# Performance work log

Hardware: AMD Instinct MI355X
Metric: run time of the kernel (lower is better)

Reference implementation:

```python
import jax, jax.numpy as jnp
import numpy as np

EPS = 1e-5

def rmsnorm(x, g):
    var = jnp.mean(jnp.square(x), axis=-1, keepdims=True)
    return x * jax.lax.rsqrt(var + EPS) * g

def setup_inputs() -> dict:
    key = jax.random.key(0)
    ks = jax.random.split(key, 8)
    B, S, T, D = 2, 2048, 2048, 1024
    H, HKV, HD = 16, 4, 64
    std = 0.02
    return {
        "x": jax.random.normal(ks[0], (B, S, D), jnp.float32),
        "kv": jax.random.normal(ks[1], (B, T, D), jnp.float32),
        "wq": jax.random.normal(ks[2], (H * HD, D), jnp.float32) * std,
        "wk": jax.random.normal(ks[3], (HKV * HD, D), jnp.float32) * std,
        "wv": jax.random.normal(ks[4], (HKV * HD, D), jnp.float32) * std,
        "wo": jax.random.normal(ks[5], (D, H * HD), jnp.float32) * std,
        "gq": jnp.ones((D,), jnp.float32),
        "gkv": jnp.ones((D,), jnp.float32),
    }

def reference(x, kv, wq, wk, wv, wo, gq, gkv):
    B, S, D = x.shape
    T = kv.shape[1]
    H, HKV, HD = 16, 4, 64
    R = H // HKV  # heads per kv group
    xn = rmsnorm(x, gq)
    kvn = rmsnorm(kv, gkv)
    # projections
    q = (xn @ wq.T).reshape(B, S, HKV, R, HD)   # grouped query heads
    k = (kvn @ wk.T).reshape(B, T, HKV, HD)
    v = (kvn @ wv.T).reshape(B, T, HKV, HD)
    scale = 1.0 / jnp.sqrt(jnp.float32(HD))
    # block-mask is None -> full dense cross attention; GQA via broadcast einsum
    scores = jnp.einsum('bsgrd,btgd->bgrst', q, k) * scale  # [B,HKV,R,S,T]
    probs = jax.nn.softmax(scores, axis=-1)
    out = jnp.einsum('bgrst,btgd->bsgrd', probs, v)  # [B,S,HKV,R,HD]
    out = out.reshape(B, S, H * HD) @ wo.T
    return x + out
```

## Files before the change

### kernel.cpp

```cpp
#include <hip/hip_runtime.h>

#define DEV __device__ __forceinline__

typedef __attribute__((ext_vector_type(8))) _Float16 h8;
typedef __attribute__((ext_vector_type(4))) float f32x4;

DEV unsigned short f2h(float f) {
  union { _Float16 h[2]; unsigned short u[2]; } v;
  v.h[0] = (_Float16)f;
  return v.u[0];
}

DEV float h2f(unsigned short u) {
  union { _Float16 h[2]; unsigned short u[2]; } v;
  v.u[0] = u;
  return (float)v.h[0];
}

DEV unsigned int pack2h(float a, float b) {
  union { __fp16 __attribute__((ext_vector_type(2))) p; unsigned int u; } v;
  v.p = __builtin_amdgcn_cvt_pkrtz(a, b);
  return v.u;
}

DEV void async_load16(const void* g, void* l) {
  __builtin_amdgcn_global_load_lds(
      (const __attribute__((address_space(1))) void*)g,
      (__attribute__((address_space(3))) void*)l,
      16, 0, 0);
}

__global__ __launch_bounds__(256) void prep(const float* __restrict__ x,
                                            const float* __restrict__ kv,
                                            const float* __restrict__ wq,
                                            const float* __restrict__ wk,
                                            const float* __restrict__ wv,
                                            const float* __restrict__ wo,
                                            const float* __restrict__ gq,
                                            const float* __restrict__ gkv,
                                            unsigned short* __restrict__ wqb,
                                            unsigned short* __restrict__ wkvb,
                                            unsigned short* __restrict__ wob,
                                            unsigned short* __restrict__ xn,
                                            unsigned short* __restrict__ kvn,
                                            float qscale) {
  const int b = blockIdx.x, tid = threadIdx.x;
  if (b < 2560) {
    const float* src;
    unsigned short* dst;
    float sc = 1.0f;
    int base;
    if (b < 1024) { src = wq; dst = wqb; sc = qscale; base = b; }
    else if (b < 1280) { src = wk; dst = wkvb; base = b - 1024; }
    else if (b < 1536) { src = wv; dst = wkvb + 262144; base = b - 1280; }
    else { src = wo; dst = wob; base = b - 1536; }
    const int i = (base * 256 + tid) * 4;
    float4 v = *(const float4*)&src[i];
    ushort4 o;
    o.x = f2h(v.x * sc); o.y = f2h(v.y * sc);
    o.z = f2h(v.z * sc); o.w = f2h(v.w * sc);
    *(ushort4*)&dst[i] = o;
    return;
  }
  int row = b - 2560;
  const float* src;
  const float* g;
  unsigned short* dst;
  if (row < 4096) { src = x; g = gq; dst = xn; }
  else { row -= 4096; src = kv; g = gkv; dst = kvn; }
  const float* xr = src + (size_t)row * 1024;
  float4 v = *(const float4*)&xr[tid * 4];
  float ss = v.x * v.x + v.y * v.y + v.z * v.z + v.w * v.w;
  ss += __shfl_xor(ss, 32); ss += __shfl_xor(ss, 16);
  ss += __shfl_xor(ss, 8);  ss += __shfl_xor(ss, 4);
  ss += __shfl_xor(ss, 2);  ss += __shfl_xor(ss, 1);
  __shared__ float red[4];
  if ((tid & 63) == 0) red[tid >> 6] = ss;
  __syncthreads();
  float tot = red[0] + red[1] + red[2] + red[3];
  float inv = rsqrtf(tot * (1.0f / 1024.0f) + 1e-5f);
  float4 gv = *(const float4*)&g[tid * 4];
  ushort4 o;
  o.x = f2h(v.x * inv * gv.x); o.y = f2h(v.y * inv * gv.y);
  o.z = f2h(v.z * inv * gv.z); o.w = f2h(v.w * inv * gv.w);
  *(ushort4*)&dst[(size_t)row * 1024 + tid * 4] = o;
}

#define GEMM_KLOOP(A_, W_, m0_, n0_, Al_, Bl_, acc_)                                   \
  for (int kk = 0; kk < 1024; kk += 64) {                                              \
    __syncthreads();                                                                   \
    _Pragma("unroll") for (int j = 0; j < 6; ++j) {                                    \
      const int idx = w * 6 + j;                                                       \
      if (idx < 16) {                                                                  \
        const int p = idx >> 3, rb = (idx & 7) * 16;                                   \
        async_load16(A_ + (size_t)(m0_ + rb + r4) * 1024 + kk + p * 32 + c4,           \
                     &Al_[p][rb * 32]);                                                \
      } else {                                                                         \
        const int ib = idx - 16;                                                       \
        const int p = ib >> 2, rb = (ib & 3) * 16;                                     \
        async_load16(W_ + (size_t)(n0_ + rb + r4) * 1024 + kk + p * 32 + c4,           \
                     &Bl_[p][rb * 32]);                                                \
      }                                                                                \
    }                                                                                  \
    __syncthreads();                                                                   \
    _Pragma("unroll") for (int kc = 0; kc < 2; ++kc) {                                 \
      h8 af[4], bf[2];                                                                 \
      _Pragma("unroll") for (int mi = 0; mi < 4; ++mi)                                 \
        af[mi] = *(const h8*)&Al_[kc][(wm0 + mi * 16 + ln) * 32 + quad * 8];           \
      _Pragma("unroll") for (int ni = 0; ni < 2; ++ni)                                 \
        bf[ni] = *(const h8*)&Bl_[kc][(wn0 + ni * 16 + ln) * 32 + quad * 8];           \
      _Pragma("unroll") for (int mi = 0; mi < 4; ++mi)                                 \
        _Pragma("unroll") for (int ni = 0; ni < 2; ++ni)                               \
          acc_[mi][ni] =                                                               \
              __builtin_amdgcn_mfma_f32_16x16x32_f16(af[mi], bf[ni], acc_[mi][ni],     \
                                                     0, 0, 0);                         \
    }                                                                                  \
  }

__global__ __launch_bounds__(256) void proj_gemm(const unsigned short* __restrict__ xn,
                                                 const unsigned short* __restrict__ kvn,
                                                 const unsigned short* __restrict__ wqb,
                                                 const unsigned short* __restrict__ wkvb,
                                                 unsigned short* __restrict__ qb,
                                                 unsigned short* __restrict__ kb,
                                                 unsigned short* __restrict__ vTb) {
  __shared__ unsigned short Al[2][128 * 32];
  __shared__ unsigned short Bl[2][64 * 32];
  const int tid = threadIdx.x;
  const int w = tid >> 6, l = tid & 63;
  const int quad = l >> 4, ln = l & 15;
  const int wm0 = (w >> 1) * 64, wn0 = (w & 1) * 32;
  const int r4 = l >> 2;
  const int c4 = (l & 3) * 8;

  int z = blockIdx.x;
  const unsigned short *A, *W;
  int m0, n0, isq;
  if (z < 512) { A = xn; W = wqb; m0 = (z >> 4) * 128; n0 = (z & 15) * 64; isq = 1; }
  else { z -= 512; A = kvn; W = wkvb; m0 = (z >> 3) * 128; n0 = (z & 7) * 64; isq = 0; }

  f32x4 acc[4][2] = {};
  GEMM_KLOOP(A, W, m0, n0, Al, Bl, acc)

#pragma unroll
  for (int mi = 0; mi < 4; ++mi)
#pragma unroll
    for (int ni = 0; ni < 2; ++ni)
#pragma unroll
      for (int r = 0; r < 4; ++r) {
        const int row = m0 + wm0 + mi * 16 + quad * 4 + r;
        const int col = n0 + wn0 + ni * 16 + ln;
        const unsigned short v = f2h(acc[mi][ni][r]);
        if (isq) {
          qb[((size_t)row << 10) + col] = v;
        } else if (col < 256) {
          kb[(size_t)row * 256 + col] = v;
        } else {
          const int c2 = col - 256, gg = c2 >> 6, dd = c2 & 63;
          const int bb = row >> 11, t = row & 2047;
          vTb[((size_t)((bb * 4 + gg) * 64 + dd) << 11) + t] = v;
        }
      }
}

__global__ __launch_bounds__(256) void o_gemm(const unsigned short* __restrict__ attb,
                                              const unsigned short* __restrict__ wob,
                                              const float* __restrict__ x,
                                              float* __restrict__ out) {
  __shared__ unsigned short Al[2][128 * 32];
  __shared__ unsigned short Bl[2][64 * 32];
  const int tid = threadIdx.x;
  const int w = tid >> 6, l = tid & 63;
  const int quad = l >> 4, ln = l & 15;
  const int wm0 = (w >> 1) * 64, wn0 = (w & 1) * 32;
  const int r4 = l >> 2;
  const int c4 = (l & 3) * 8;

  const int m0 = (blockIdx.x >> 4) * 128, n0 = (blockIdx.x & 15) * 64;

  f32x4 acc[4][2] = {};
  GEMM_KLOOP(attb, wob, m0, n0, Al, Bl, acc)

#pragma unroll
  for (int mi = 0; mi < 4; ++mi)
#pragma unroll
    for (int ni = 0; ni < 2; ++ni)
#pragma unroll
      for (int r = 0; r < 4; ++r) {
        const int row = m0 + wm0 + mi * 16 + quad * 4 + r;
        const int col = n0 + wn0 + ni * 16 + ln;
        const size_t idx = ((size_t)row << 10) + col;
        out[idx] = x[idx] + acc[mi][ni][r];
      }
}

__global__ __launch_bounds__(256, 4) void flash_attn(const unsigned short* __restrict__ q,
                                                     const unsigned short* __restrict__ k,
                                                     const unsigned short* __restrict__ vT,
                                                     unsigned short* __restrict__ o0,
                                                     unsigned short* __restrict__ o1,
                                                     float* __restrict__ l0p,
                                                     float* __restrict__ l1p) {
  __shared__ unsigned short KV[4][64 * 32];
  __shared__ unsigned short P[4 * 32 * 72];

  const int tid = threadIdx.x;
  const int w = tid >> 6, l = tid & 63;
  const int quad = l >> 4, ln = l & 15;
  const int s0 = blockIdx.x * 128;
  const int h = blockIdx.y, g = h >> 2;
  const int b = blockIdx.z >> 1, ts = blockIdx.z & 1;
  const int tbase = ts << 10;

  unsigned short* Opart = ts ? o1 : o0;
  float* lpart = ts ? l1p : l0p;

  h8 qf[2][2];
#pragma unroll
  for (int nq = 0; nq < 2; ++nq)
#pragma unroll
    for (int c = 0; c < 2; ++c)
      qf[nq][c] = *(const h8*)&q[(((size_t)(b * 2048 + s0 + w * 32 + nq * 16 + ln)) << 10) +
                                 h * 64 + c * 32 + quad * 8];

  f32x4 oacc[2][4] = {};
  float lsum[2] = {0.0f, 0.0f};

  const unsigned short* kbase = k + ((size_t)(b * 2048)) * 256 + g * 64;
  const unsigned short* vbase = vT + (((size_t)(b * 4 + g) * 64) << 11);
  unsigned short* Pw = &P[w * 32 * 72];

  const int r4 = l >> 2;
  const int c4 = (l & 3) * 8;

  for (int it = 0; it < 16; ++it) {
    const int t0 = tbase + it * 64;
    __syncthreads();
#pragma unroll
    for (int c = 0; c < 4; ++c) {
      const unsigned short* src;
      if (w < 2)
        src = kbase + (size_t)(t0 + c * 16 + r4) * 256 + w * 32 + c4;
      else
        src = vbase + (((size_t)(c * 16 + r4)) << 11) + t0 + (w - 2) * 32 + c4;
      async_load16(src, &KV[w][c * 512]);
    }
    __syncthreads();

    f32x4 st[2][4];
#pragma unroll
    for (int tb = 0; tb < 4; ++tb) {
      h8 ka = *(const h8*)&KV[0][(tb * 16 + ln) * 32 + quad * 8];
      h8 kb2 = *(const h8*)&KV[1][(tb * 16 + ln) * 32 + quad * 8];
#pragma unroll
      for (int nq = 0; nq < 2; ++nq) {
        f32x4 s = {};
        s = __builtin_amdgcn_mfma_f32_16x16x32_f16(ka, qf[nq][0], s, 0, 0, 0);
        s = __builtin_amdgcn_mfma_f32_16x16x32_f16(kb2, qf[nq][1], s, 0, 0, 0);
        st[nq][tb] = s;
      }
    }

#pragma unroll
    for (int nq = 0; nq < 2; ++nq) {
#pragma unroll
      for (int tb = 0; tb < 4; ++tb) {
        float p0 = __builtin_amdgcn_exp2f(fminf(st[nq][tb][0], 14.0f));
        float p1 = __builtin_amdgcn_exp2f(fminf(st[nq][tb][1], 14.0f));
        float p2 = __builtin_amdgcn_exp2f(fminf(st[nq][tb][2], 14.0f));
        float p3 = __builtin_amdgcn_exp2f(fminf(st[nq][tb][3], 14.0f));
        lsum[nq] += (p0 + p1) + (p2 + p3);
        uint2 pk; pk.x = pack2h(p0, p1); pk.y = pack2h(p2, p3);
        *(uint2*)&Pw[(nq * 16 + ln) * 72 + tb * 16 + quad * 4] = pk;
      }
    }

    asm volatile("s_waitcnt lgkmcnt(0)" ::: "memory");

#pragma unroll
    for (int c = 0; c < 2; ++c) {
      h8 pf0 = *(const h8*)&Pw[(0 * 16 + ln) * 72 + c * 32 + quad * 8];
      h8 pf1 = *(const h8*)&Pw[(1 * 16 + ln) * 72 + c * 32 + quad * 8];
#pragma unroll
      for (int cb = 0; cb < 4; ++cb) {
        h8 vb = *(const h8*)&KV[2 + c][(cb * 16 + ln) * 32 + quad * 8];
        oacc[0][cb] = __builtin_amdgcn_mfma_f32_16x16x32_f16(pf0, vb, oacc[0][cb], 0, 0, 0);
        oacc[1][cb] = __builtin_amdgcn_mfma_f32_16x16x32_f16(pf1, vb, oacc[1][cb], 0, 0, 0);
      }
    }
  }

#pragma unroll
  for (int nq = 0; nq < 2; ++nq) {
    lsum[nq] += __shfl_xor(lsum[nq], 16);
    lsum[nq] += __shfl_xor(lsum[nq], 32);
    if (l < 16)
      lpart[(size_t)(b * 2048 + s0 + w * 32 + nq * 16 + l) * 16 + h] = lsum[nq];
#pragma unroll
    for (int r = 0; r < 4; ++r) {
      const size_t row = (size_t)(b * 2048 + s0 + w * 32 + nq * 16 + quad * 4 + r);
#pragma unroll
      for (int cb = 0; cb < 4; ++cb)
        Opart[(row << 10) + h * 64 + cb * 16 + ln] = f2h(oacc[nq][cb][r]);
    }
  }
}

__global__ __launch_bounds__(256) void combine(const unsigned short* __restrict__ O0,
                                               const unsigned short* __restrict__ O1,
                                               const float* __restrict__ l0p,
                                               const float* __restrict__ l1p,
                                               unsigned short* __restrict__ att) {
  const int row = blockIdx.x, tid = threadIdx.x;
  const int col = tid * 4;
  const int h = tid >> 4;
  const float inv = 1.0f / (l0p[row * 16 + h] + l1p[row * 16 + h]);
  const size_t idx = ((size_t)row << 10) + col;
  ushort4 a = *(const ushort4*)&O0[idx];
  ushort4 b = *(const ushort4*)&O1[idx];
  ushort4 o;
  o.x = f2h((h2f(a.x) + h2f(b.x)) * inv);
  o.y = f2h((h2f(a.y) + h2f(b.y)) * inv);
  o.z = f2h((h2f(a.z) + h2f(b.z)) * inv);
  o.w = f2h((h2f(a.w) + h2f(b.w)) * inv);
  *(ushort4*)&att[idx] = o;
}

extern "C" void kernel_launch(void* const* d_in, const int* in_sizes, int n_in,
                              void* d_out, int out_size, void* d_ws, size_t ws_size,
                              hipStream_t stream) {
  const float* x   = (const float*)d_in[0];
  const float* kv  = (const float*)d_in[1];
  const float* wq  = (const float*)d_in[2];
  const float* wk  = (const float*)d_in[3];
  const float* wv  = (const float*)d_in[4];
  const float* wo  = (const float*)d_in[5];
  const float* gq  = (const float*)d_in[6];
  const float* gkv = (const float*)d_in[7];

  char* ws = (char*)d_ws;
  unsigned short* xn   = (unsigned short*)(ws);
  unsigned short* kvn  = (unsigned short*)(ws + 8388608);
  unsigned short* qb   = (unsigned short*)(ws + 16777216);
  unsigned short* kb   = (unsigned short*)(ws + 25165824);
  unsigned short* vTb  = (unsigned short*)(ws + 27262976);
  unsigned short* attb = (unsigned short*)(ws + 29360128);
  unsigned short* wqb  = (unsigned short*)(ws + 37748736);
  unsigned short* wkvb = (unsigned short*)(ws + 39845888);
  unsigned short* wob  = (unsigned short*)(ws + 40894464);
  unsigned short* Opart0 = xn;
  unsigned short* Opart1 = kvn;
  float* l0p = (float*)wqb;
  float* l1p = (float*)(ws + 37748736 + 262144);

  const float qscale = 0.18033688011112042f;

  prep<<<10752, 256, 0, stream>>>(x, kv, wq, wk, wv, wo, gq, gkv,
                                  wqb, wkvb, wob, xn, kvn, qscale);

  proj_gemm<<<768, 256, 0, stream>>>(xn, kvn, wqb, wkvb, qb, kb, vTb);

  flash_attn<<<dim3(16, 16, 4), 256, 0, stream>>>(qb, kb, vTb, Opart0, Opart1, l0p, l1p);
  combine<<<4096, 256, 0, stream>>>(Opart0, Opart1, l0p, l1p, attb);

  o_gemm<<<512, 256, 0, stream>>>(attb, wob, x, (float*)d_out);
}
```

Before: 200.9 us.

## XOR-swizzle LDS tiles and group GEMM block order for L2 reuse

Applies an XOR swizzle to the 16-byte chunk column used when async-loading GEMM and attention K/V tiles into LDS, and applies the matching swizzle on the MFMA fragment reads. The aim is to cut LDS bank conflicts on the 64-byte-stride row layout. Separately, the projection and output GEMMs remap block indices so groups of 8 consecutive blocks share N tiles across adjacent M tiles, improving L2 reuse. The swizzle must match exactly between writer and reader lanes, so any mismatch would corrupt the results.

```diff
diff --git a/kernel.cpp b/kernel.cpp
--- a/kernel.cpp
+++ b/kernel.cpp
@@ -29,6 +29,7 @@
       (__attribute__((address_space(3))) void*)l,
       16, 0, 0);
 }
+
 
 __global__ __launch_bounds__(256) void prep(const float* __restrict__ x,
                                             const float* __restrict__ kv,
@@ -93,12 +94,12 @@
       const int idx = w * 6 + j;                                                       \
       if (idx < 16) {                                                                  \
         const int p = idx >> 3, rb = (idx & 7) * 16;                                   \
-        async_load16(A_ + (size_t)(m0_ + rb + r4) * 1024 + kk + p * 32 + c4,           \
+        async_load16(A_ + (size_t)(m0_ + rb + r4) * 1024 + kk + p * 32 + c4s,          \
                      &Al_[p][rb * 32]);                                                \
       } else {                                                                         \
         const int ib = idx - 16;                                                       \
         const int p = ib >> 2, rb = (ib & 3) * 16;                                     \
-        async_load16(W_ + (size_t)(n0_ + rb + r4) * 1024 + kk + p * 32 + c4,           \
+        async_load16(W_ + (size_t)(n0_ + rb + r4) * 1024 + kk + p * 32 + c4s,          \
                      &Bl_[p][rb * 32]);                                                \
       }                                                                                \
     }                                                                                  \
@@ -106,9 +107,9 @@
     _Pragma("unroll") for (int kc = 0; kc < 2; ++kc) {                                 \
       h8 af[4], bf[2];                                                                 \
       _Pragma("unroll") for (int mi = 0; mi < 4; ++mi)                                 \
-        af[mi] = *(const h8*)&Al_[kc][(wm0 + mi * 16 + ln) * 32 + quad * 8];           \
+        af[mi] = *(const h8*)&Al_[kc][(wm0 + mi * 16 + ln) * 32 + qs8];                \
       _Pragma("unroll") for (int ni = 0; ni < 2; ++ni)                                 \
-        bf[ni] = *(const h8*)&Bl_[kc][(wn0 + ni * 16 + ln) * 32 + quad * 8];           \
+        bf[ni] = *(const h8*)&Bl_[kc][(wn0 + ni * 16 + ln) * 32 + qs8];                \
       _Pragma("unroll") for (int mi = 0; mi < 4; ++mi)                                 \
         _Pragma("unroll") for (int ni = 0; ni < 2; ++ni)                               \
           acc_[mi][ni] =                                                               \
@@ -131,13 +132,21 @@
   const int quad = l >> 4, ln = l & 15;
   const int wm0 = (w >> 1) * 64, wn0 = (w & 1) * 32;
   const int r4 = l >> 2;
-  const int c4 = (l & 3) * 8;
+  const int c4s = (((l & 3) ^ ((l >> 3) & 3))) * 8;
+  const int qs8 = (quad ^ ((l >> 1) & 3)) * 8;
 
   int z = blockIdx.x;
   const unsigned short *A, *W;
   int m0, n0, isq;
-  if (z < 512) { A = xn; W = wqb; m0 = (z >> 4) * 128; n0 = (z & 15) * 64; isq = 1; }
-  else { z -= 512; A = kvn; W = wkvb; m0 = (z >> 3) * 128; n0 = (z & 7) * 64; isq = 0; }
+  if (z < 512) {
+    A = xn; W = wqb; isq = 1;
+    m0 = (((z >> 7) << 3) + (z & 7)) * 128;
+    n0 = ((z >> 3) & 15) * 64;
+  } else {
+    z -= 512; A = kvn; W = wkvb; isq = 0;
+    m0 = (((z >> 6) << 3) + (z & 7)) * 128;
+    n0 = ((z >> 3) & 7) * 64;
+  }
 
   f32x4 acc[4][2] = {};
   GEMM_KLOOP(A, W, m0, n0, Al, Bl, acc)
@@ -174,9 +183,12 @@
   const int quad = l >> 4, ln = l & 15;
   const int wm0 = (w >> 1) * 64, wn0 = (w & 1) * 32;
   const int r4 = l >> 2;
-  const int c4 = (l & 3) * 8;
-
-  const int m0 = (blockIdx.x >> 4) * 128, n0 = (blockIdx.x & 15) * 64;
+  const int c4s = (((l & 3) ^ ((l >> 3) & 3))) * 8;
+  const int qs8 = (quad ^ ((l >> 1) & 3)) * 8;
+
+  const int z = blockIdx.x;
+  const int m0 = (((z >> 7) << 3) + (z & 7)) * 128;
+  const int n0 = ((z >> 3) & 15) * 64;
 
   f32x4 acc[4][2] = {};
   GEMM_KLOOP(attb, wob, m0, n0, Al, Bl, acc)
@@ -231,7 +243,8 @@
   unsigned short* Pw = &P[w * 32 * 72];
 
   const int r4 = l >> 2;
-  const int c4 = (l & 3) * 8;
+  const int c4s = (((l & 3) ^ ((l >> 3) & 3))) * 8;
+  const int qs8 = (quad ^ ((l >> 1) & 3)) * 8;
 
   for (int it = 0; it < 16; ++it) {
     const int t0 = tbase + it * 64;
@@ -240,9 +253,9 @@
     for (int c = 0; c < 4; ++c) {
       const unsigned short* src;
       if (w < 2)
-        src = kbase + (size_t)(t0 + c * 16 + r4) * 256 + w * 32 + c4;
+        src = kbase + (size_t)(t0 + c * 16 + r4) * 256 + w * 32 + c4s;
       else
-        src = vbase + (((size_t)(c * 16 + r4)) << 11) + t0 + (w - 2) * 32 + c4;
+        src = vbase + (((size_t)(c * 16 + r4)) << 11) + t0 + (w - 2) * 32 + c4s;
       async_load16(src, &KV[w][c * 512]);
     }
     __syncthreads();
@@ -250,8 +263,8 @@
     f32x4 st[2][4];
 #pragma unroll
     for (int tb = 0; tb < 4; ++tb) {
-      h8 ka = *(const h8*)&KV[0][(tb * 16 + ln) * 32 + quad * 8];
-      h8 kb2 = *(const h8*)&KV[1][(tb * 16 + ln) * 32 + quad * 8];
+      h8 ka = *(const h8*)&KV[0][tb * 512 + ln * 32 + qs8];
+      h8 kb2 = *(const h8*)&KV[1][tb * 512 + ln * 32 + qs8];
 #pragma unroll
       for (int nq = 0; nq < 2; ++nq) {
         f32x4 s = {};
@@ -283,7 +296,7 @@
       h8 pf1 = *(const h8*)&Pw[(1 * 16 + ln) * 72 + c * 32 + quad * 8];
 #pragma unroll
       for (int cb = 0; cb < 4; ++cb) {
-        h8 vb = *(const h8*)&KV[2 + c][(cb * 16 + ln) * 32 + quad * 8];
+        h8 vb = *(const h8*)&KV[2 + c][cb * 512 + ln * 32 + qs8];
         oacc[0][cb] = __builtin_amdgcn_mfma_f32_16x16x32_f16(pf0, vb, oacc[0][cb], 0, 0, 0);
         oacc[1][cb] = __builtin_amdgcn_mfma_f32_16x16x32_f16(pf1, vb, oacc[1][cb], 0, 0, 0);
       }
```

Measured after the change: 194.5 us. 1.03x faster.
